# Optimization experiments

Measured on AMD Instinct MI355X. Metric: run time of the kernel, lower is better.

Reference implementation:

```python
import jax, jax.numpy as jnp
import numpy as np

K = 5          # number of neighbors (self excluded)
EPS = 1e-7     # distance epsilon
Q = 0.98       # quantile for radius normalization


def _cdist(A):
    # Euclidean pairwise distances [N, N] via the matmul expansion.
    sq = jnp.sum(A * A, axis=-1)
    d2 = sq[:, None] + sq[None, :] - 2.0 * (A @ A.T)
    return jnp.sqrt(jnp.maximum(d2, 0.0))


def _lid(values):
    # values: [N, K] ascending neighbor distances; LID via log-distance ratios.
    norm = values[:, -1:]
    return -jnp.sum(jnp.log10(values) - jnp.log10(norm), axis=1)


def setup_inputs() -> dict:
    key = jax.random.key(0)
    k1, k2 = jax.random.split(key)
    X = jax.random.normal(k1, (8192, 256), dtype=jnp.float32)
    Z = jax.random.normal(k2, (8192, 64), dtype=jnp.float32)
    return {"X": X, "Z": Z}


def reference(X, Z):
    n = X.shape[0]
    normA1 = jnp.quantile(jnp.linalg.norm(X - jnp.mean(X, axis=0), axis=1), Q)
    normA2 = jnp.quantile(jnp.linalg.norm(Z - jnp.mean(Z, axis=0), axis=1), Q)

    # k-NN in X space (drop self at column 0)
    x_dist = (_cdist(X) + EPS) / normA1
    neg_vals, idx = jax.lax.top_k(-x_dist, K + 1)   # smallest K+1, ascending
    values = (-neg_vals)[:, 1:]
    nn_mask = idx[:, 1:]
    lid_X = _lid(values)

    # gather the SAME neighbor indices in Z space
    z_dist = (_cdist(Z) + EPS) / normA2
    extracted = jnp.take_along_axis(z_dist, nn_mask, axis=1)
    lid_Z = _lid(extracted)

    return jnp.sum(jnp.square(lid_X - lid_Z)) / (n * K * 10)
```

## Files before the change

kernel.cpp:

```cpp
#include <hip/hip_runtime.h>
#include <math.h>
#include <stdint.h>

#define EPS     1e-7f
#define NR      8192
#define DX      256
#define DZ      64
#define KNN     5
#define KEEP    6
#define NSPLIT  8
#define NPOOL   (NSPLIT * KEEP)
#define NCAND   16
#define JS      (NR / NSPLIT)
#define JT      64
#define NCHUNK  (JS / JT)
#define RBLK    64
#define SC1     0x7F7F7F7F
#define BIASF   256.0f

typedef float f32x4 __attribute__((ext_vector_type(4)));
typedef int   i32x8 __attribute__((ext_vector_type(8)));

__device__ __forceinline__ uint32_t umin_(uint32_t a, uint32_t b) { return a < b ? a : b; }
__device__ __forceinline__ uint32_t umax_(uint32_t a, uint32_t b) { return a < b ? b : a; }

__device__ __forceinline__ uint32_t to_e4m3(float f) {
    const uint32_t u = __float_as_uint(f);
    const uint32_t s = (u >> 24) & 0x80u;
    const int e = (int)((u >> 23) & 0xFFu) - 127;
    if (e < -10) return s;
    if (e > 8)   return s | 0x7Eu;
    const uint32_t mant = (u & 0x7FFFFFu) | 0x800000u;
    const int shift = (e < -6) ? (14 - e) : 20;
    uint32_t q = (mant + (1u << (shift - 1))) >> shift;
    int E = (e < -6) ? 0 : (e + 7);
    if (q >= 16) { q >>= 1; E += 1; }
    if (E == 0) return s | q;
    return s | ((uint32_t)E << 3) | (q & 7u);
}

__global__ __launch_bounds__(256) void split_k(const float* __restrict__ X,
                                               uint8_t* __restrict__ Xq,
                                               float* __restrict__ sqX,
                                               float* __restrict__ out) {
    if (blockIdx.x == 0 && threadIdx.x == 0) out[0] = 0.0f;
    const int row  = blockIdx.x * 4 + (threadIdx.x >> 6);
    const int lane = threadIdx.x & 63;
    const float4 v = *(const float4*)&X[(size_t)row * DX + lane * 4];
    float s = v.x * v.x + v.y * v.y + v.z * v.z + v.w * v.w;
    const uint32_t b = to_e4m3(v.x) | (to_e4m3(v.y) << 8) |
                       (to_e4m3(v.z) << 16) | (to_e4m3(v.w) << 24);
    ((uint32_t*)Xq)[(size_t)row * (DX / 4) + lane] = b;
    #pragma unroll
    for (int o = 32; o > 0; o >>= 1) s += __shfl_down(s, o);
    if (lane == 0) sqX[row] = s;
}

#define FOLD_BODY(KILL)                                                                   \
    _Pragma("unroll")                                                                     \
    for (int g = 0; g < 2; ++g) {                                                         \
        _Pragma("unroll")                                                                 \
        for (int r = 0; r < 4; ++r) {                                                     \
            const int q = g * 4 + r;                                                      \
            uint32_t c0 = (__float_as_uint(acc[0][g][r]) & 0xFFFFE000u) | (uint32_t)j0;   \
            uint32_t c1 = (__float_as_uint(acc[1][g][r]) & 0xFFFFE000u) | (uint32_t)(j0 + 16); \
            if (KILL) {                                                                   \
                const int irow = rowbase + g * 16 + quad * 4 + r;                         \
                c0 = (j0 == irow)      ? 0xFFFFFFFFu : c0;                                \
                c1 = (j0 + 16 == irow) ? 0xFFFFFFFFu : c1;                                \
            }                                                                             \
            const uint32_t lo = umin_(c0, c1);                                            \
            const uint32_t hi = umax_(c0, c1);                                            \
            const uint32_t b0 = best[q][0], b1 = best[q][1], b2 = best[q][2],             \
                           b3 = best[q][3], b4 = best[q][4];                              \
            best[q][0] = umin_(b0, lo);                                                   \
            best[q][1] = umin_(umin_(b1, umax_(b0, lo)), hi);                             \
            best[q][2] = umin_(umin_(b2, umax_(b1, lo)), umax_(b0, hi));                  \
            best[q][3] = umin_(umin_(b3, umax_(b2, lo)), umax_(b1, hi));                  \
            best[q][4] = umin_(umin_(b4, umax_(b3, lo)), umax_(b2, hi));                  \
        }                                                                                 \
    }

__global__ __launch_bounds__(256, 2) void mfma_topk_k(const uint8_t* __restrict__ Xq,
                                                      const float* __restrict__ sqX,
                                                      uint32_t* __restrict__ partials) {
    __shared__ __align__(16) uint8_t smem[16384];
    __shared__ uint32_t mb2[RBLK][2][KNN];
    __shared__ __align__(16) float sq_s[JS];
    const uint4* Bv = (const uint4*)smem;

    const int tid  = threadIdx.x;
    const int w    = tid >> 6;
    const int lane = tid & 63;
    const int n    = lane & 15;
    const int quad = lane >> 4;
    const int x7   = n & 7;
    const int h    = w >> 1;
    const int sp   = w & 1;
    const int s    = blockIdx.x & 7;
    const int ib   = (blockIdx.x >> 3) * RBLK;
    const int jb0  = s * JS;
    const int rowbase = ib + h * 32;

    ((f32x4*)sq_s)[tid] = ((const f32x4*)(sqX + jb0))[tid];

    const int rel   = rowbase - jb0;
    const int cdiag = __builtin_amdgcn_readfirstlane((rel >= 0 && rel < JS) ? (rel >> 6) : -1);

    i32x8 Aq[2][2];
    #pragma unroll
    for (int g = 0; g < 2; ++g)
        #pragma unroll
        for (int kf = 0; kf < 2; ++kf)
            Aq[g][kf] = *(const i32x8*)(Xq + (size_t)(rowbase + g * 16 + n) * DX
                                        + kf * 128 + quad * 32);

    uint32_t best[8][KNN];
    #pragma unroll
    for (int q = 0; q < 8; ++q)
        #pragma unroll
        for (int k = 0; k < KNN; ++k) best[q][k] = 0xFFFFFFFFu;

    int srcoff[4];
    #pragma unroll
    for (int u = 0; u < 4; ++u) {
        const int q  = w * 256 + u * 64 + lane;
        const int sj = q >> 4;
        const int c  = (q & 15) ^ (sj & 7);
        srcoff[u] = sj * DX + c * 16;
    }

    for (int jc = 0; jc < NCHUNK; ++jc) {
        const int jb = jb0 + jc * JT;
        __syncthreads();
        #pragma unroll
        for (int u = 0; u < 4; ++u) {
            const uint8_t* src = Xq + (size_t)jb * DX + srcoff[u];
            uint8_t* dst = smem + (size_t)(w * 256 + u * 64) * 16;
            __builtin_amdgcn_global_load_lds((const __attribute__((address_space(1))) uint32_t*)src,
                                             (__attribute__((address_space(3))) uint32_t*)dst,
                                             16, 0, 0);
        }
        __syncthreads();

        const int   sqb  = jc * JT + sp * 32 + n;
        const float ini0 = fmaf(-0.5f, sq_s[sqb],      -BIASF);
        const float ini1 = fmaf(-0.5f, sq_s[sqb + 16], -BIASF);

        f32x4 acc[2][2];
        #pragma unroll
        for (int g = 0; g < 2; ++g)
            #pragma unroll
            for (int r = 0; r < 4; ++r) { acc[0][g][r] = ini0; acc[1][g][r] = ini1; }

        #pragma unroll
        for (int kf = 0; kf < 2; ++kf) {
            #pragma unroll
            for (int si = 0; si < 2; ++si) {
                const int sj = (sp * 2 + si) * 16 + n;
                const int cb = kf * 8 + quad * 2;
                const uint4 p0 = Bv[sj * 16 + (cb ^ x7)];
                const uint4 p1 = Bv[sj * 16 + ((cb + 1) ^ x7)];
                i32x8 b;
                b[0] = p0.x; b[1] = p0.y; b[2] = p0.z; b[3] = p0.w;
                b[4] = p1.x; b[5] = p1.y; b[6] = p1.z; b[7] = p1.w;
                acc[si][0] = __builtin_amdgcn_mfma_scale_f32_16x16x128_f8f6f4(
                                 Aq[0][kf], b, acc[si][0], 0, 0, 0, SC1, 0, SC1);
                acc[si][1] = __builtin_amdgcn_mfma_scale_f32_16x16x128_f8f6f4(
                                 Aq[1][kf], b, acc[si][1], 0, 0, 0, SC1, 0, SC1);
            }
        }

        const int j0 = jb + sp * 32 + n;
        if (jc != cdiag) {
            FOLD_BODY(0)
        } else {
            FOLD_BODY(1)
        }
    }

    #pragma unroll
    for (int q = 0; q < 8; ++q) {
        uint32_t a0 = best[q][0], a1 = best[q][1], a2 = best[q][2],
                 a3 = best[q][3], a4 = best[q][4];
        #pragma unroll
        for (int mask = 1; mask <= 8; mask <<= 1) {
            const uint32_t b0 = __shfl_xor(a0, mask);
            const uint32_t b1 = __shfl_xor(a1, mask);
            const uint32_t b2 = __shfl_xor(a2, mask);
            const uint32_t b3 = __shfl_xor(a3, mask);
            const uint32_t b4 = __shfl_xor(a4, mask);
            const uint32_t c0 = umin_(a0, b0);
            const uint32_t c1 = umin_(umin_(a1, b1), umax_(a0, b0));
            const uint32_t c2 = umin_(umin_(a2, b2), umin_(umax_(a0, b1), umax_(a1, b0)));
            const uint32_t c3 = umin_(umin_(a3, b3),
                                      umin_(umax_(a1, b1), umin_(umax_(a0, b2), umax_(a2, b0))));
            const uint32_t c4 = umin_(umin_(a4, b4),
                                      umin_(umin_(umax_(a0, b3), umax_(a1, b2)),
                                            umin_(umax_(a2, b1), umax_(a3, b0))));
            a0 = c0; a1 = c1; a2 = c2; a3 = c3; a4 = c4;
        }
        const int rloc = h * 32 + (q >> 2) * 16 + quad * 4 + (q & 3);
        uint32_t v = a0;
        v = (n == 1) ? a1 : v;
        v = (n == 2) ? a2 : v;
        v = (n == 3) ? a3 : v;
        v = (n == 4) ? a4 : v;
        if (n < KNN) mb2[rloc][sp][n] = v;
    }
    __syncthreads();

    if (tid < RBLK) {
        const uint32_t a0 = mb2[tid][0][0], a1 = mb2[tid][0][1], a2 = mb2[tid][0][2],
                       a3 = mb2[tid][0][3], a4 = mb2[tid][0][4];
        const uint32_t b0 = mb2[tid][1][0], b1 = mb2[tid][1][1], b2 = mb2[tid][1][2],
                       b3 = mb2[tid][1][3], b4 = mb2[tid][1][4];
        uint32_t o[KEEP];
        o[0] = umin_(a0, b0);
        o[1] = umin_(umin_(a1, b1), umax_(a0, b0));
        o[2] = umin_(umin_(a2, b2), umin_(umax_(a0, b1), umax_(a1, b0)));
        o[3] = umin_(umin_(a3, b3), umin_(umax_(a1, b1), umin_(umax_(a0, b2), umax_(a2, b0))));
        o[4] = umin_(umin_(a4, b4), umin_(umin_(umax_(a0, b3), umax_(a1, b2)),
                                          umin_(umax_(a2, b1), umax_(a3, b0))));
        o[5] = umin_(umin_(umax_(a0, b4), umax_(a4, b0)),
                     umin_(umax_(a1, b3), umin_(umax_(a2, b2), umax_(a3, b1))));
        #pragma unroll
        for (int k = 0; k < KEEP; ++k)
            partials[(size_t)(ib + tid) * NPOOL + s * KEEP + k] = o[k];
    }
}

__global__ __launch_bounds__(256) void finalize_k(const uint32_t* __restrict__ parts,
                                                  const float* __restrict__ X,
                                                  const float* __restrict__ Z,
                                                  const float* __restrict__ sqX,
                                                  float* __restrict__ out) {
    __shared__ float wsum[4];
    const int wv   = threadIdx.x >> 6;
    const int lane = threadIdx.x & 63;
    const int i    = blockIdx.x * 4 + wv;

    uint32_t v = (lane < NPOOL) ? parts[(size_t)i * NPOOL + lane] : 0xFFFFFFFFu;
    #pragma unroll
    for (int kk = 2; kk <= 64; kk <<= 1) {
        #pragma unroll
        for (int jj = kk >> 1; jj > 0; jj >>= 1) {
            const uint32_t o = __shfl_xor(v, jj);
            const bool keepmin = ((lane & kk) == 0) == ((lane & jj) == 0);
            v = keepmin ? umin_(v, o) : umax_(v, o);
        }
    }

    const float4 xi = *(const float4*)(X + (size_t)i * DX + lane * 4);

    float p[16];
    #pragma unroll
    for (int c = 0; c < NCAND; ++c) {
        const int jc = (int)(__shfl(v, c) & 0x1FFFu);
        const float4 xj = *(const float4*)(X + (size_t)jc * DX + lane * 4);
        p[c] = fmaf(xi.x, xj.x, fmaf(xi.y, xj.y, fmaf(xi.z, xj.z, xi.w * xj.w)));
    }
    #pragma unroll
    for (int c = 0; c < NCAND; ++c) {
        p[c] += __shfl_xor(p[c], 1);
        p[c] += __shfl_xor(p[c], 2);
        p[c] += __shfl_xor(p[c], 4);
        p[c] += __shfl_xor(p[c], 8);
    }
    const int cs = lane & 15;
    float dotv = p[0];
    dotv = (cs == 1)  ? p[1]  : dotv;
    dotv = (cs == 2)  ? p[2]  : dotv;
    dotv = (cs == 3)  ? p[3]  : dotv;
    dotv = (cs == 4)  ? p[4]  : dotv;
    dotv = (cs == 5)  ? p[5]  : dotv;
    dotv = (cs == 6)  ? p[6]  : dotv;
    dotv = (cs == 7)  ? p[7]  : dotv;
    dotv = (cs == 8)  ? p[8]  : dotv;
    dotv = (cs == 9)  ? p[9]  : dotv;
    dotv = (cs == 10) ? p[10] : dotv;
    dotv = (cs == 11) ? p[11] : dotv;
    dotv = (cs == 12) ? p[12] : dotv;
    dotv = (cs == 13) ? p[13] : dotv;
    dotv = (cs == 14) ? p[14] : dotv;
    dotv = (cs == 15) ? p[15] : dotv;
    dotv += __shfl_xor(dotv, 16);
    dotv += __shfl_xor(dotv, 32);

    unsigned long long k16 = 0xFFFFFFFFFFFFFFFFull;
    const int jl = (int)(v & 0x1FFFu);
    if (lane < NCAND) {
        const float d2x = (sqX[i] + sqX[jl]) - 2.0f * dotv;
        k16 = ((unsigned long long)__float_as_uint(d2x) << 32) | (unsigned)jl;
    }
    #pragma unroll
    for (int kk = 2; kk <= 16; kk <<= 1) {
        #pragma unroll
        for (int jj = kk >> 1; jj > 0; jj >>= 1) {
            const unsigned long long o = __shfl_xor(k16, jj);
            const bool keepmin = ((lane & kk) == 0) == ((lane & jj) == 0);
            k16 = keepmin ? (k16 < o ? k16 : o) : (k16 < o ? o : k16);
        }
    }

    const float d2k = __uint_as_float((uint32_t)(k16 >> 32));
    const int   jk  = (int)(k16 & 0x1FFFull);
    float lkx = 0.0f;
    if (lane < KNN) lkx = log10f(sqrtf(fmaxf(d2k, 0.0f)) + EPS);
    const float l4x = __shfl(lkx, KNN - 1);
    float sx = lkx;
    sx += __shfl_xor(sx, 1);
    sx += __shfl_xor(sx, 2);
    sx += __shfl_xor(sx, 4);

    const float zi = Z[(size_t)i * DZ + lane];
    float zsum = 0.0f, l4z = 0.0f;
    #pragma unroll
    for (int k = 0; k < KNN; ++k) {
        const int jz = __shfl(jk, k);
        const float zj = Z[(size_t)jz * DZ + lane];
        const float d = zi - zj;
        float s = d * d;
        s += __shfl_xor(s, 1);
        s += __shfl_xor(s, 2);
        s += __shfl_xor(s, 4);
        s += __shfl_xor(s, 8);
        s += __shfl_xor(s, 16);
        s += __shfl_xor(s, 32);
        const float lk = log10f(sqrtf(fmaxf(s, 0.0f)) + EPS);
        zsum += lk;
        if (k == KNN - 1) l4z = lk;
    }

    if (lane == 0) {
        const float lx = -(__shfl(sx, 0) - (float)KNN * l4x);
        const float lz = -(zsum - (float)KNN * l4z);
        const float diff = lx - lz;
        wsum[wv] = diff * diff * (1.0f / ((float)NR * KNN * 10.0f));
    }
    __syncthreads();
    if (threadIdx.x == 0)
        atomicAdd(out, wsum[0] + wsum[1] + wsum[2] + wsum[3]);
}

extern "C" void kernel_launch(void* const* d_in, const int* in_sizes, int n_in,
                              void* d_out, int out_size, void* d_ws, size_t ws_size,
                              hipStream_t stream) {
    const float* X = (const float*)d_in[0];
    const float* Z = (const float*)d_in[1];
    float* out = (float*)d_out;

    char* ws = (char*)d_ws;
    float*     sqX      = (float*)ws;
    uint32_t*  partials = (uint32_t*)(ws + 32768);
    uint8_t*   Xq       = (uint8_t*)(ws + 32768 + 2097152);

    split_k<<<NR / 4, 256, 0, stream>>>(X, Xq, sqX, out);
    mfma_topk_k<<<(NR / RBLK) * NSPLIT, 256, 0, stream>>>(Xq, sqX, partials);
    finalize_k<<<NR / 4, 256, 0, stream>>>(partials, X, Z, sqX, out);
}
```

Measured before the change: 141.3 us.

## Skip top-k merge when candidates lose, precompute LDS and global addresses

The fold step now runs the sorted-insert network only when the smaller candidate beats the current fifth-best, so per-lane compare work is skipped once the running lists have settled. LDS read indices and global source pointers are computed once before the loop and advanced incrementally, which removes per-iteration integer address math. The launch bounds are rewritten as explicit flat-workgroup and waves-per-EU attributes. The new branch adds divergence inside the wave and a compare on every step, which may cost more than the skipped min/max chain.

```diff
diff --git a/kernel.cpp b/kernel.cpp
--- a/kernel.cpp
+++ b/kernel.cpp
@@ -63,27 +63,30 @@
         for (int r = 0; r < 4; ++r) {                                                     \
             const int q = g * 4 + r;                                                      \
             uint32_t c0 = (__float_as_uint(acc[0][g][r]) & 0xFFFFE000u) | (uint32_t)j0;   \
-            uint32_t c1 = (__float_as_uint(acc[1][g][r]) & 0xFFFFE000u) | (uint32_t)(j0 + 16); \
+            uint32_t c1 = (__float_as_uint(acc[1][g][r]) & 0xFFFFE000u) | (uint32_t)j1;   \
             if (KILL) {                                                                   \
                 const int irow = rowbase + g * 16 + quad * 4 + r;                         \
-                c0 = (j0 == irow)      ? 0xFFFFFFFFu : c0;                                \
-                c1 = (j0 + 16 == irow) ? 0xFFFFFFFFu : c1;                                \
+                c0 = (j0 == irow) ? 0xFFFFFFFFu : c0;                                     \
+                c1 = (j1 == irow) ? 0xFFFFFFFFu : c1;                                     \
             }                                                                             \
             const uint32_t lo = umin_(c0, c1);                                            \
             const uint32_t hi = umax_(c0, c1);                                            \
-            const uint32_t b0 = best[q][0], b1 = best[q][1], b2 = best[q][2],             \
-                           b3 = best[q][3], b4 = best[q][4];                              \
-            best[q][0] = umin_(b0, lo);                                                   \
-            best[q][1] = umin_(umin_(b1, umax_(b0, lo)), hi);                             \
-            best[q][2] = umin_(umin_(b2, umax_(b1, lo)), umax_(b0, hi));                  \
-            best[q][3] = umin_(umin_(b3, umax_(b2, lo)), umax_(b1, hi));                  \
-            best[q][4] = umin_(umin_(b4, umax_(b3, lo)), umax_(b2, hi));                  \
+            if (lo < best[q][4]) {      \
+                const uint32_t b0 = best[q][0], b1 = best[q][1], b2 = best[q][2],         \
+                               b3 = best[q][3], b4 = best[q][4];                          \
+                best[q][0] = umin_(b0, lo);                                               \
+                best[q][1] = umin_(umin_(b1, umax_(b0, lo)), hi);                         \
+                best[q][2] = umin_(umin_(b2, umax_(b1, lo)), umax_(b0, hi));              \
+                best[q][3] = umin_(umin_(b3, umax_(b2, lo)), umax_(b1, hi));              \
+                best[q][4] = umin_(umin_(b4, umax_(b3, lo)), umax_(b2, hi));              \
+            }                                                                             \
         }                                                                                 \
     }
 
-__global__ __launch_bounds__(256, 2) void mfma_topk_k(const uint8_t* __restrict__ Xq,
-                                                      const float* __restrict__ sqX,
-                                                      uint32_t* __restrict__ partials) {
+__global__ __attribute__((amdgpu_flat_work_group_size(256, 256), amdgpu_waves_per_eu(2, 2)))
+void mfma_topk_k(const uint8_t* __restrict__ Xq,
+                 const float* __restrict__ sqX,
+                 uint32_t* __restrict__ partials) {
     __shared__ __align__(16) uint8_t smem[16384];
     __shared__ uint32_t mb2[RBLK][2][KNN];
     __shared__ __align__(16) float sq_s[JS];
@@ -121,31 +124,42 @@
         #pragma unroll
         for (int k = 0; k < KNN; ++k) best[q][k] = 0xFFFFFFFFu;
 
-    int srcoff[4];
+    const uint8_t* srcp[4];
+    uint8_t*       dstp[4];
     #pragma unroll
     for (int u = 0; u < 4; ++u) {
         const int q  = w * 256 + u * 64 + lane;
         const int sj = q >> 4;
         const int c  = (q & 15) ^ (sj & 7);
-        srcoff[u] = sj * DX + c * 16;
-    }
+        srcp[u] = Xq + (size_t)jb0 * DX + sj * DX + c * 16;
+        dstp[u] = smem + (size_t)(w * 256 + u * 64) * 16;
+    }
+    int bidx[2][2][2];
+    #pragma unroll
+    for (int kf = 0; kf < 2; ++kf)
+        #pragma unroll
+        for (int si = 0; si < 2; ++si) {
+            const int sj = (sp * 2 + si) * 16 + n;
+            const int cb = kf * 8 + quad * 2;
+            bidx[kf][si][0] = sj * 16 + (cb ^ x7);
+            bidx[kf][si][1] = sj * 16 + ((cb + 1) ^ x7);
+        }
+    const float* sqp = sq_s + sp * 32 + n;
+    int j0 = jb0 + sp * 32 + n;
 
     for (int jc = 0; jc < NCHUNK; ++jc) {
-        const int jb = jb0 + jc * JT;
         __syncthreads();
         #pragma unroll
         for (int u = 0; u < 4; ++u) {
-            const uint8_t* src = Xq + (size_t)jb * DX + srcoff[u];
-            uint8_t* dst = smem + (size_t)(w * 256 + u * 64) * 16;
-            __builtin_amdgcn_global_load_lds((const __attribute__((address_space(1))) uint32_t*)src,
-                                             (__attribute__((address_space(3))) uint32_t*)dst,
+            __builtin_amdgcn_global_load_lds((const __attribute__((address_space(1))) uint32_t*)srcp[u],
+                                             (__attribute__((address_space(3))) uint32_t*)dstp[u],
                                              16, 0, 0);
+            srcp[u] += JT * DX;
         }
         __syncthreads();
 
-        const int   sqb  = jc * JT + sp * 32 + n;
-        const float ini0 = fmaf(-0.5f, sq_s[sqb],      -BIASF);
-        const float ini1 = fmaf(-0.5f, sq_s[sqb + 16], -BIASF);
+        const float ini0 = fmaf(-0.5f, sqp[jc * JT],      -BIASF);
+        const float ini1 = fmaf(-0.5f, sqp[jc * JT + 16], -BIASF);
 
         f32x4 acc[2][2];
         #pragma unroll
@@ -157,26 +171,23 @@
         for (int kf = 0; kf < 2; ++kf) {
             #pragma unroll
             for (int si = 0; si < 2; ++si) {
-                const int sj = (sp * 2 + si) * 16 + n;
-                const int cb = kf * 8 + quad * 2;
-                const uint4 p0 = Bv[sj * 16 + (cb ^ x7)];
-                const uint4 p1 = Bv[sj * 16 + ((cb + 1) ^ x7)];
-                i32x8 b;
-                b[0] = p0.x; b[1] = p0.y; b[2] = p0.z; b[3] = p0.w;
-                b[4] = p1.x; b[5] = p1.y; b[6] = p1.z; b[7] = p1.w;
+                union { uint4 p[2]; i32x8 v; } bb;
+                bb.p[0] = Bv[bidx[kf][si][0]];
+                bb.p[1] = Bv[bidx[kf][si][1]];
                 acc[si][0] = __builtin_amdgcn_mfma_scale_f32_16x16x128_f8f6f4(
-                                 Aq[0][kf], b, acc[si][0], 0, 0, 0, SC1, 0, SC1);
+                                 Aq[0][kf], bb.v, acc[si][0], 0, 0, 0, SC1, 0, SC1);
                 acc[si][1] = __builtin_amdgcn_mfma_scale_f32_16x16x128_f8f6f4(
-                                 Aq[1][kf], b, acc[si][1], 0, 0, 0, SC1, 0, SC1);
+                                 Aq[1][kf], bb.v, acc[si][1], 0, 0, 0, SC1, 0, SC1);
             }
         }
 
-        const int j0 = jb + sp * 32 + n;
+        const int j1 = j0 + 16;
         if (jc != cdiag) {
             FOLD_BODY(0)
         } else {
             FOLD_BODY(1)
         }
+        j0 += JT;
     }
 
     #pragma unroll
```

After: 147.7 us. 1.05x slower.
